# Performance work log

Hardware: AMD Instinct MI355X
Metric: run time of the kernel (lower is better)

## Reference

```python
import jax, jax.numpy as jnp
import numpy as np

B, V, D, H, E = 512, 128, 256, 4, 2
Dh = D // H

def setup_inputs() -> dict:
    key = jax.random.key(0)
    k = jax.random.split(key, 8)
    x = jax.random.normal(k[0], (B, V, D), dtype=jnp.float32)
    adj = jax.random.randint(k[1], (V, V), 0, 2, dtype=jnp.int32)
    adj = adj.at[jnp.arange(V), jnp.arange(V)].set(1)  # self loops so no empty columns for real nodes
    edge_attr = jax.random.normal(k[2], (V, V, E), dtype=jnp.float32)
    mask = jax.random.bernoulli(k[3], 0.1, (B, V))  # True = padded view
    # learned params (torch Linear: y = x @ W.T)
    W = jax.random.normal(k[4], (D, D), dtype=jnp.float32) / np.sqrt(D)
    a = jax.random.normal(k[5], (2 * Dh,), dtype=jnp.float32) / np.sqrt(2 * Dh)  # attn.weight flattened
    Ew = jax.random.normal(k[6], (H, E), dtype=jnp.float32) / np.sqrt(E)  # edge_proj.weight
    return {"x": x, "adj": adj, "edge_attr": edge_attr, "mask": mask, "W": W, "a": a, "Ew": Ew}

def reference(x, adj, edge_attr, mask, W, a, Ew):
    Bv, Vv, Dv = x.shape
    Hh = Ew.shape[0]
    Dhh = Dv // Hh
    Wx = (x @ W.T).reshape(Bv, Vv, Hh, Dhh)                 # [B,V,H,Dh]
    a_src, a_dst = a[:Dhh], a[Dhh:]
    s_src = jnp.einsum('bvhd,d->bvh', Wx, a_src)             # a^T[Wh_i ; .]
    s_dst = jnp.einsum('bvhd,d->bvh', Wx, a_dst)             # a^T[. ; Wh_j]
    ef = jnp.einsum('ije,he->ijh', edge_attr, Ew)            # [V,V,H]
    e = s_src[:, :, None, :] + s_dst[:, None, :, :] + ef[None]  # [B,i,j,H]
    e = jnp.where(e >= 0, e, 0.2 * e)                        # leaky_relu(0.2)
    valid = (adj.astype(bool))[None, :, :, None] & (~mask)[:, :, None, None] & (~mask)[:, None, :, None]
    e = jnp.where(valid, e, -jnp.inf)
    # softmax over source dim i (axis=1), safe for all-masked columns (-> 0, like nan_to_num)
    m = jnp.max(e, axis=1, keepdims=True)
    m = jnp.where(jnp.isfinite(m), m, 0.0)
    p = jnp.where(valid, jnp.exp(e - m), 0.0)
    denom = jnp.sum(p, axis=1, keepdims=True)
    alpha = p / jnp.where(denom == 0, 1.0, denom)            # [B,i,j,H]
    h = jnp.einsum('bijh,bihd->bjhd', alpha, Wx).reshape(Bv, Vv, Dv)
    h = jax.nn.elu(h)
    return jnp.where(mask[:, :, None], 0.0, h)
```

## Files before the change

kernel.cpp:

```cpp
#include <hip/hip_runtime.h>
#include <cmath>

#define BB 512
#define VV 128
#define DD 256
#define HH 4
#define DHH 64

typedef unsigned short u16;
typedef __attribute__((ext_vector_type(8))) short bf16x8;
typedef __attribute__((ext_vector_type(4))) short bf16x4;
typedef __attribute__((ext_vector_type(4))) float f32x4;

__device__ __forceinline__ u16 f2bf(float f) {
    unsigned u = __builtin_bit_cast(unsigned, f);
    u = (u + 0x7fffu + ((u >> 16) & 1u)) >> 16;
    return (u16)u;
}

__global__ void k_ef(const float* __restrict__ ea, const float* __restrict__ Ew,
                     const int* __restrict__ adj, float* __restrict__ efm) {
    int idx = blockIdx.x * 256 + threadIdx.x;
    int hh = idx >> 14, ij = idx & 16383;
    float v = -INFINITY;
    if (adj[ij])
        v = fmaf(ea[ij * 2 + 1], Ew[hh * 2 + 1], ea[ij * 2] * Ew[hh * 2]);
    efm[idx] = v;
}

__global__ __launch_bounds__(256, 2) void k_gemm(
    const float* __restrict__ x, const float* __restrict__ Wm,
    const float* __restrict__ a, u16* __restrict__ WxT,
    float* __restrict__ s_src, float* __restrict__ s_dst) {
    __shared__ u16 As[128 * 32];
    __shared__ u16 Bs[128 * 32];

    const int t = threadIdx.x;
    const int w = t >> 6, L = t & 63;
    const int wr = w >> 1, wc = w & 1;
    const int lr = L & 15, lg = L >> 4;
    const int b  = blockIdx.x;
    const int c0 = blockIdx.y * 128;
    const int row = t >> 1, seg = t & 1;

    f32x4 acc[4][4];
    #pragma unroll
    for (int i = 0; i < 4; ++i)
        #pragma unroll
        for (int j = 0; j < 4; ++j) acc[i][j] = (f32x4){0.f, 0.f, 0.f, 0.f};

    const float* xrow = x  + (size_t)(b * 128 + row) * DD + seg * 16;
    const float* wrow = Wm + (size_t)(c0 + row) * DD + seg * 16;
    u16* adst = &As[row * 32 + seg * 16];
    u16* bdst = &Bs[row * 32 + seg * 16];

    for (int k0 = 0; k0 < DD; k0 += 32) {
        float4 f0 = *(const float4*)(xrow + k0);
        float4 f1 = *(const float4*)(xrow + k0 + 4);
        float4 f2 = *(const float4*)(xrow + k0 + 8);
        float4 f3 = *(const float4*)(xrow + k0 + 12);
        float4 g0 = *(const float4*)(wrow + k0);
        float4 g1 = *(const float4*)(wrow + k0 + 4);
        float4 g2 = *(const float4*)(wrow + k0 + 8);
        float4 g3 = *(const float4*)(wrow + k0 + 12);
        bf16x8 pa, pb, qa, qb;
        pa[0]=(short)f2bf(f0.x); pa[1]=(short)f2bf(f0.y); pa[2]=(short)f2bf(f0.z); pa[3]=(short)f2bf(f0.w);
        pa[4]=(short)f2bf(f1.x); pa[5]=(short)f2bf(f1.y); pa[6]=(short)f2bf(f1.z); pa[7]=(short)f2bf(f1.w);
        pb[0]=(short)f2bf(f2.x); pb[1]=(short)f2bf(f2.y); pb[2]=(short)f2bf(f2.z); pb[3]=(short)f2bf(f2.w);
        pb[4]=(short)f2bf(f3.x); pb[5]=(short)f2bf(f3.y); pb[6]=(short)f2bf(f3.z); pb[7]=(short)f2bf(f3.w);
        qa[0]=(short)f2bf(g0.x); qa[1]=(short)f2bf(g0.y); qa[2]=(short)f2bf(g0.z); qa[3]=(short)f2bf(g0.w);
        qa[4]=(short)f2bf(g1.x); qa[5]=(short)f2bf(g1.y); qa[6]=(short)f2bf(g1.z); qa[7]=(short)f2bf(g1.w);
        qb[0]=(short)f2bf(g2.x); qb[1]=(short)f2bf(g2.y); qb[2]=(short)f2bf(g2.z); qb[3]=(short)f2bf(g2.w);
        qb[4]=(short)f2bf(g3.x); qb[5]=(short)f2bf(g3.y); qb[6]=(short)f2bf(g3.z); qb[7]=(short)f2bf(g3.w);
        *(bf16x8*)adst       = pa;
        *(bf16x8*)(adst + 8) = pb;
        *(bf16x8*)bdst       = qa;
        *(bf16x8*)(bdst + 8) = qb;
        __syncthreads();

        bf16x8 af[4], bfr[4];
        #pragma unroll
        for (int mi = 0; mi < 4; ++mi)
            af[mi] = *(const bf16x8*)&As[(wr * 64 + mi * 16 + lr) * 32 + lg * 8];
        #pragma unroll
        for (int ni = 0; ni < 4; ++ni)
            bfr[ni] = *(const bf16x8*)&Bs[(wc * 64 + ni * 16 + lr) * 32 + lg * 8];
        #pragma unroll
        for (int mi = 0; mi < 4; ++mi)
            #pragma unroll
            for (int ni = 0; ni < 4; ++ni)
                acc[mi][ni] = __builtin_amdgcn_mfma_f32_16x16x32_bf16(
                    af[mi], bfr[ni], acc[mi][ni], 0, 0, 0);
        __syncthreads();
    }

    const int h = blockIdx.y * 2 + wc;
    float as_[4], ad_[4];
    #pragma unroll
    for (int ni = 0; ni < 4; ++ni) {
        as_[ni] = a[ni * 16 + lr];
        ad_[ni] = a[64 + ni * 16 + lr];
    }
    float ps[16], pd[16];
    #pragma unroll
    for (int k = 0; k < 16; ++k) { ps[k] = 0.f; pd[k] = 0.f; }

    #pragma unroll
    for (int mi = 0; mi < 4; ++mi) {
        #pragma unroll
        for (int ni = 0; ni < 4; ++ni) {
            int d  = ni * 16 + lr;
            int vb = wr * 64 + mi * 16 + lg * 4;
            bf16x4 o;
            #pragma unroll
            for (int r = 0; r < 4; ++r) {
                float v = acc[mi][ni][r];
                o[r] = (short)f2bf(v);
                ps[mi * 4 + r] = fmaf(v, as_[ni], ps[mi * 4 + r]);
                pd[mi * 4 + r] = fmaf(v, ad_[ni], pd[mi * 4 + r]);
            }
            *(bf16x4*)&WxT[(((size_t)b * HH + h) * DHH + d) * VV + vb] = o;
        }
    }
    #pragma unroll
    for (int k = 0; k < 16; ++k) {
        #pragma unroll
        for (int m = 1; m < 16; m <<= 1) {
            ps[k] += __shfl_xor(ps[k], m);
            pd[k] += __shfl_xor(pd[k], m);
        }
    }
    if (lr == 0) {
        #pragma unroll
        for (int mi = 0; mi < 4; ++mi)
            #pragma unroll
            for (int r = 0; r < 4; ++r) {
                int v = wr * 64 + mi * 16 + lg * 4 + r;
                s_src[((size_t)b * VV + v) * HH + h] = ps[mi * 4 + r];
                s_dst[((size_t)b * VV + v) * HH + h] = pd[mi * 4 + r];
            }
    }
}

__global__ __launch_bounds__(256, 4) void k_attn(
    const u16* __restrict__ WxT, const float* __restrict__ s_src,
    const float* __restrict__ s_dst, const float* __restrict__ efm,
    const int* __restrict__ mask, float* __restrict__ out) {
    __shared__ u16 alT[128 * 136];
    __shared__ float ssl[128], sdl[128], red[256], rden[128];

    const int t = threadIdx.x;
    const int b = blockIdx.x >> 2, h = blockIdx.x & 3;

    if (t < 128) {
        int mk = mask[b * VV + t];
        float vs = s_src[((size_t)b * VV + t) * HH + h];
        float vd = s_dst[((size_t)b * VV + t) * HH + h];
        ssl[t] = mk ? -INFINITY : vs;
        sdl[t] = mk ? -INFINITY : vd;
    }
    __syncthreads();

    const int j = t & 127, half = t >> 7;
    const float sdj = sdl[j];
    const float* efh = efm + ((size_t)h * VV + half * 64) * VV + j;
    float psum = 0.f;
    for (int i8 = 0; i8 < 64; i8 += 8) {
        bf16x8 pk;
        #pragma unroll
        for (int u = 0; u < 8; ++u) {
            int i = half * 64 + i8 + u;
            float e = ssl[i] + sdj + efh[(size_t)(i8 + u) * VV];
            e = e >= 0.f ? e : 0.2f * e;
            float p = __expf(e);
            psum += p;
            pk[u] = (short)f2bf(p);
        }
        *(bf16x8*)&alT[j * 136 + half * 64 + i8] = pk;
    }
    red[half * 128 + j] = psum;
    __syncthreads();
    if (half == 0) {
        float s = red[j] + red[128 + j];
        rden[j] = s > 0.f ? 1.f / s : 0.f;
    }
    __syncthreads();

    const int w = t >> 6, L = t & 63;
    const int lr = L & 15, lg = L >> 4;
    const u16* gB = WxT + ((size_t)b * HH + h) * DHH * VV;
    f32x4 acc[2][4];
    #pragma unroll
    for (int mi = 0; mi < 2; ++mi)
        #pragma unroll
        for (int ni = 0; ni < 4; ++ni) acc[mi][ni] = (f32x4){0.f, 0.f, 0.f, 0.f};

    #pragma unroll
    for (int ks = 0; ks < 4; ++ks) {
        const int kk = ks * 32 + lg * 8;
        bf16x8 bfr[4];
        #pragma unroll
        for (int ni = 0; ni < 4; ++ni)
            bfr[ni] = *(const bf16x8*)(gB + (size_t)(ni * 16 + lr) * VV + kk);
        #pragma unroll
        for (int mi = 0; mi < 2; ++mi) {
            bf16x8 af = *(const bf16x8*)&alT[(w * 32 + mi * 16 + lr) * 136 + kk];
            #pragma unroll
            for (int ni = 0; ni < 4; ++ni)
                acc[mi][ni] = __builtin_amdgcn_mfma_f32_16x16x32_bf16(
                    af, bfr[ni], acc[mi][ni], 0, 0, 0);
        }
    }

    #pragma unroll
    for (int mi = 0; mi < 2; ++mi)
        #pragma unroll
        for (int ni = 0; ni < 4; ++ni) {
            int dcol = ni * 16 + lr;
            int jb   = w * 32 + mi * 16 + lg * 4;
            float* op = out + ((size_t)b * VV + jb) * DD + h * DHH + dcol;
            #pragma unroll
            for (int r = 0; r < 4; ++r) {
                float v = acc[mi][ni][r] * rden[jb + r];
                v = v > 0.f ? v : expm1f(v);
                op[(size_t)r * DD] = v;
            }
        }
}

extern "C" void kernel_launch(void* const* d_in, const int* in_sizes, int n_in,
                              void* d_out, int out_size, void* d_ws, size_t ws_size,
                              hipStream_t stream) {
    const float* x    = (const float*)d_in[0];
    const int*   adj  = (const int*)d_in[1];
    const float* ea   = (const float*)d_in[2];
    const int*   mask = (const int*)d_in[3];
    const float* Wm   = (const float*)d_in[4];
    const float* a    = (const float*)d_in[5];
    const float* Ew   = (const float*)d_in[6];
    float* out = (float*)d_out;

    u16*   WxT   = (u16*)d_ws;
    float* s_src = (float*)(WxT + (size_t)BB * HH * DHH * VV);
    float* s_dst = s_src + (size_t)BB * VV * HH;
    float* efm   = s_dst + (size_t)BB * VV * HH;

    k_ef<<<HH * VV * VV / 256, 256, 0, stream>>>(ea, Ew, adj, efm);
    k_gemm<<<dim3(BB, 2), 256, 0, stream>>>(x, Wm, a, WxT, s_src, s_dst);
    k_attn<<<BB * HH, 256, 0, stream>>>(WxT, s_src, s_dst, efm, mask, out);
}
```

Before: 168.5 us.

## Fuse projection GEMM and attention into one kernel keeping Wx in LDS

Merges the projection GEMM and the attention kernel into one kernel per (batch, head-pair). The bf16 Wx tile and the attention scores now stay in shared memory instead of going through global memory, which removes the WxT/s_src/s_dst global round trip and one launch. It also register-prefetches the next K slice of x/W during the MFMA loop and pads the LDS rows (stride 40) to reduce bank conflicts. The cost is much larger LDS use per block (about 70KB), which may limit occupancy, and fewer blocks (1024 instead of 2048) for the attention phase.

```diff
diff --git a/kernel.cpp b/kernel.cpp
--- a/kernel.cpp
+++ b/kernel.cpp
@@ -16,6 +16,9 @@
     unsigned u = __builtin_bit_cast(unsigned, f);
     u = (u + 0x7fffu + ((u >> 16) & 1u)) >> 16;
     return (u16)u;
+}
+__device__ __forceinline__ unsigned pk2(float a, float b) {
+    return (unsigned)f2bf(a) | ((unsigned)f2bf(b) << 16);
 }
 
 __global__ void k_ef(const float* __restrict__ ea, const float* __restrict__ Ew,
@@ -28,20 +31,32 @@
     efm[idx] = v;
 }
 
-__global__ __launch_bounds__(256, 2) void k_gemm(
+__global__ __launch_bounds__(256, 2) void k_fused(
     const float* __restrict__ x, const float* __restrict__ Wm,
-    const float* __restrict__ a, u16* __restrict__ WxT,
-    float* __restrict__ s_src, float* __restrict__ s_dst) {
-    __shared__ u16 As[128 * 32];
-    __shared__ u16 Bs[128 * 32];
+    const float* __restrict__ a, const float* __restrict__ efm,
+    const int* __restrict__ mask, float* __restrict__ out) {
+    __shared__ u16 WxL[128 * 136];
+    __shared__ u16 scratch[128 * 136];
+    __shared__ float ssl[256], sdl[256], red[256], rden[128];
+    __shared__ int mkl[128];
+
+    u16* As = scratch;
+    u16* Bs = scratch + 128 * 40;
+    u16* alT = scratch;
 
     const int t = threadIdx.x;
+    const int b = blockIdx.x, hp = blockIdx.y;
     const int w = t >> 6, L = t & 63;
     const int wr = w >> 1, wc = w & 1;
     const int lr = L & 15, lg = L >> 4;
-    const int b  = blockIdx.x;
-    const int c0 = blockIdx.y * 128;
+
+    if (t < 128) mkl[t] = mask[b * VV + t];
+
     const int row = t >> 1, seg = t & 1;
+    const float* xs = x  + ((size_t)b * VV + row) * DD + seg * 16;
+    const float* ws = Wm + ((size_t)(hp * 128 + row)) * DD + seg * 16;
+    u16* adst = As + row * 40 + seg * 16;
+    u16* bdst = Bs + row * 40 + seg * 16;
 
     f32x4 acc[4][4];
     #pragma unroll
@@ -49,42 +64,44 @@
         #pragma unroll
         for (int j = 0; j < 4; ++j) acc[i][j] = (f32x4){0.f, 0.f, 0.f, 0.f};
 
-    const float* xrow = x  + (size_t)(b * 128 + row) * DD + seg * 16;
-    const float* wrow = Wm + (size_t)(c0 + row) * DD + seg * 16;
-    u16* adst = &As[row * 32 + seg * 16];
-    u16* bdst = &Bs[row * 32 + seg * 16];
-
-    for (int k0 = 0; k0 < DD; k0 += 32) {
-        float4 f0 = *(const float4*)(xrow + k0);
-        float4 f1 = *(const float4*)(xrow + k0 + 4);
-        float4 f2 = *(const float4*)(xrow + k0 + 8);
-        float4 f3 = *(const float4*)(xrow + k0 + 12);
-        float4 g0 = *(const float4*)(wrow + k0);
-        float4 g1 = *(const float4*)(wrow + k0 + 4);
-        float4 g2 = *(const float4*)(wrow + k0 + 8);
-        float4 g3 = *(const float4*)(wrow + k0 + 12);
-        bf16x8 pa, pb, qa, qb;
-        pa[0]=(short)f2bf(f0.x); pa[1]=(short)f2bf(f0.y); pa[2]=(short)f2bf(f0.z); pa[3]=(short)f2bf(f0.w);
-        pa[4]=(short)f2bf(f1.x); pa[5]=(short)f2bf(f1.y); pa[6]=(short)f2bf(f1.z); pa[7]=(short)f2bf(f1.w);
-        pb[0]=(short)f2bf(f2.x); pb[1]=(short)f2bf(f2.y); pb[2]=(short)f2bf(f2.z); pb[3]=(short)f2bf(f2.w);
-        pb[4]=(short)f2bf(f3.x); pb[5]=(short)f2bf(f3.y); pb[6]=(short)f2bf(f3.z); pb[7]=(short)f2bf(f3.w);
-        qa[0]=(short)f2bf(g0.x); qa[1]=(short)f2bf(g0.y); qa[2]=(short)f2bf(g0.z); qa[3]=(short)f2bf(g0.w);
-        qa[4]=(short)f2bf(g1.x); qa[5]=(short)f2bf(g1.y); qa[6]=(short)f2bf(g1.z); qa[7]=(short)f2bf(g1.w);
-        qb[0]=(short)f2bf(g2.x); qb[1]=(short)f2bf(g2.y); qb[2]=(short)f2bf(g2.z); qb[3]=(short)f2bf(g2.w);
-        qb[4]=(short)f2bf(g3.x); qb[5]=(short)f2bf(g3.y); qb[6]=(short)f2bf(g3.z); qb[7]=(short)f2bf(g3.w);
-        *(bf16x8*)adst       = pa;
-        *(bf16x8*)(adst + 8) = pb;
+    float4 px[4], pw[4];
+    #pragma unroll
+    for (int q = 0; q < 4; ++q) {
+        px[q] = *(const float4*)(xs + q * 4);
+        pw[q] = *(const float4*)(ws + q * 4);
+    }
+
+    for (int ks = 0; ks < 8; ++ks) {
+        bf16x8 va, vb, qa, qb;
+        unsigned* vap = (unsigned*)&va; unsigned* vbp = (unsigned*)&vb;
+        unsigned* qap = (unsigned*)&qa; unsigned* qbp = (unsigned*)&qb;
+        vap[0] = pk2(px[0].x, px[0].y); vap[1] = pk2(px[0].z, px[0].w);
+        vap[2] = pk2(px[1].x, px[1].y); vap[3] = pk2(px[1].z, px[1].w);
+        vbp[0] = pk2(px[2].x, px[2].y); vbp[1] = pk2(px[2].z, px[2].w);
+        vbp[2] = pk2(px[3].x, px[3].y); vbp[3] = pk2(px[3].z, px[3].w);
+        qap[0] = pk2(pw[0].x, pw[0].y); qap[1] = pk2(pw[0].z, pw[0].w);
+        qap[2] = pk2(pw[1].x, pw[1].y); qap[3] = pk2(pw[1].z, pw[1].w);
+        qbp[0] = pk2(pw[2].x, pw[2].y); qbp[1] = pk2(pw[2].z, pw[2].w);
+        qbp[2] = pk2(pw[3].x, pw[3].y); qbp[3] = pk2(pw[3].z, pw[3].w);
+        *(bf16x8*)adst       = va;
+        *(bf16x8*)(adst + 8) = vb;
         *(bf16x8*)bdst       = qa;
         *(bf16x8*)(bdst + 8) = qb;
         __syncthreads();
-
+        if (ks < 7) {
+            #pragma unroll
+            for (int q = 0; q < 4; ++q) {
+                px[q] = *(const float4*)(xs + (ks + 1) * 32 + q * 4);
+                pw[q] = *(const float4*)(ws + (ks + 1) * 32 + q * 4);
+            }
+        }
         bf16x8 af[4], bfr[4];
         #pragma unroll
         for (int mi = 0; mi < 4; ++mi)
-            af[mi] = *(const bf16x8*)&As[(wr * 64 + mi * 16 + lr) * 32 + lg * 8];
+            af[mi] = *(const bf16x8*)&As[(wr * 64 + mi * 16 + lr) * 40 + lg * 8];
         #pragma unroll
         for (int ni = 0; ni < 4; ++ni)
-            bfr[ni] = *(const bf16x8*)&Bs[(wc * 64 + ni * 16 + lr) * 32 + lg * 8];
+            bfr[ni] = *(const bf16x8*)&Bs[(wc * 64 + ni * 16 + lr) * 40 + lg * 8];
         #pragma unroll
         for (int mi = 0; mi < 4; ++mi)
             #pragma unroll
@@ -94,7 +111,6 @@
         __syncthreads();
     }
 
-    const int h = blockIdx.y * 2 + wc;
     float as_[4], ad_[4];
     #pragma unroll
     for (int ni = 0; ni < 4; ++ni) {
@@ -104,13 +120,12 @@
     float ps[16], pd[16];
     #pragma unroll
     for (int k = 0; k < 16; ++k) { ps[k] = 0.f; pd[k] = 0.f; }
-
     #pragma unroll
     for (int mi = 0; mi < 4; ++mi) {
         #pragma unroll
         for (int ni = 0; ni < 4; ++ni) {
-            int d  = ni * 16 + lr;
-            int vb = wr * 64 + mi * 16 + lg * 4;
+            const int c  = wc * 64 + ni * 16 + lr;
+            const int vb = wr * 64 + mi * 16 + lg * 4;
             bf16x4 o;
             #pragma unroll
             for (int r = 0; r < 4; ++r) {
@@ -119,7 +134,7 @@
                 ps[mi * 4 + r] = fmaf(v, as_[ni], ps[mi * 4 + r]);
                 pd[mi * 4 + r] = fmaf(v, ad_[ni], pd[mi * 4 + r]);
             }
-            *(bf16x4*)&WxT[(((size_t)b * HH + h) * DHH + d) * VV + vb] = o;
+            *(bf16x4*)&WxL[c * 136 + vb] = o;
         }
     }
     #pragma unroll
@@ -136,96 +151,78 @@
             #pragma unroll
             for (int r = 0; r < 4; ++r) {
                 int v = wr * 64 + mi * 16 + lg * 4 + r;
-                s_src[((size_t)b * VV + v) * HH + h] = ps[mi * 4 + r];
-                s_dst[((size_t)b * VV + v) * HH + h] = pd[mi * 4 + r];
-            }
-    }
-}
-
-__global__ __launch_bounds__(256, 4) void k_attn(
-    const u16* __restrict__ WxT, const float* __restrict__ s_src,
-    const float* __restrict__ s_dst, const float* __restrict__ efm,
-    const int* __restrict__ mask, float* __restrict__ out) {
-    __shared__ u16 alT[128 * 136];
-    __shared__ float ssl[128], sdl[128], red[256], rden[128];
-
-    const int t = threadIdx.x;
-    const int b = blockIdx.x >> 2, h = blockIdx.x & 3;
-
-    if (t < 128) {
-        int mk = mask[b * VV + t];
-        float vs = s_src[((size_t)b * VV + t) * HH + h];
-        float vd = s_dst[((size_t)b * VV + t) * HH + h];
-        ssl[t] = mk ? -INFINITY : vs;
-        sdl[t] = mk ? -INFINITY : vd;
+                bool mk = mkl[v] != 0;
+                ssl[wc * 128 + v] = mk ? -INFINITY : ps[mi * 4 + r];
+                sdl[wc * 128 + v] = mk ? -INFINITY : pd[mi * 4 + r];
+            }
     }
     __syncthreads();
 
     const int j = t & 127, half = t >> 7;
-    const float sdj = sdl[j];
-    const float* efh = efm + ((size_t)h * VV + half * 64) * VV + j;
-    float psum = 0.f;
-    for (int i8 = 0; i8 < 64; i8 += 8) {
-        bf16x8 pk;
-        #pragma unroll
-        for (int u = 0; u < 8; ++u) {
-            int i = half * 64 + i8 + u;
-            float e = ssl[i] + sdj + efh[(size_t)(i8 + u) * VV];
-            e = e >= 0.f ? e : 0.2f * e;
-            float p = __expf(e);
-            psum += p;
-            pk[u] = (short)f2bf(p);
-        }
-        *(bf16x8*)&alT[j * 136 + half * 64 + i8] = pk;
-    }
-    red[half * 128 + j] = psum;
-    __syncthreads();
-    if (half == 0) {
-        float s = red[j] + red[128 + j];
-        rden[j] = s > 0.f ? 1.f / s : 0.f;
-    }
-    __syncthreads();
-
-    const int w = t >> 6, L = t & 63;
-    const int lr = L & 15, lg = L >> 4;
-    const u16* gB = WxT + ((size_t)b * HH + h) * DHH * VV;
-    f32x4 acc[2][4];
-    #pragma unroll
-    for (int mi = 0; mi < 2; ++mi)
-        #pragma unroll
-        for (int ni = 0; ni < 4; ++ni) acc[mi][ni] = (f32x4){0.f, 0.f, 0.f, 0.f};
-
-    #pragma unroll
-    for (int ks = 0; ks < 4; ++ks) {
-        const int kk = ks * 32 + lg * 8;
-        bf16x8 bfr[4];
-        #pragma unroll
-        for (int ni = 0; ni < 4; ++ni)
-            bfr[ni] = *(const bf16x8*)(gB + (size_t)(ni * 16 + lr) * VV + kk);
-        #pragma unroll
-        for (int mi = 0; mi < 2; ++mi) {
-            bf16x8 af = *(const bf16x8*)&alT[(w * 32 + mi * 16 + lr) * 136 + kk];
+    for (int hl = 0; hl < 2; ++hl) {
+        const int h = hp * 2 + hl;
+        const float sdj = sdl[hl * 128 + j];
+        const float* efh = efm + ((size_t)h * VV + half * 64) * VV + j;
+        u16* alrow = alT + j * 136 + half * 64;
+        float psum = 0.f;
+        for (int i8 = 0; i8 < 64; i8 += 8) {
+            bf16x8 pk;
+            #pragma unroll
+            for (int u = 0; u < 8; ++u) {
+                float e = ssl[hl * 128 + half * 64 + i8 + u] + sdj
+                        + efh[(size_t)(i8 + u) * VV];
+                e = e >= 0.f ? e : 0.2f * e;
+                float p = __expf(e);
+                psum += p;
+                pk[u] = (short)f2bf(p);
+            }
+            *(bf16x8*)(alrow + i8) = pk;
+        }
+        red[half * 128 + j] = psum;
+        __syncthreads();
+        if (half == 0) {
+            float s = red[j] + red[128 + j];
+            rden[j] = s > 0.f ? 1.f / s : 0.f;
+        }
+        __syncthreads();
+
+        f32x4 acc2[2][4];
+        #pragma unroll
+        for (int mi = 0; mi < 2; ++mi)
+            #pragma unroll
+            for (int ni = 0; ni < 4; ++ni) acc2[mi][ni] = (f32x4){0.f, 0.f, 0.f, 0.f};
+        #pragma unroll
+        for (int ks = 0; ks < 4; ++ks) {
+            const int kk = ks * 32 + lg * 8;
+            bf16x8 bfr2[4];
             #pragma unroll
             for (int ni = 0; ni < 4; ++ni)
-                acc[mi][ni] = __builtin_amdgcn_mfma_f32_16x16x32_bf16(
-                    af, bfr[ni], acc[mi][ni], 0, 0, 0);
-        }
-    }
-
-    #pragma unroll
-    for (int mi = 0; mi < 2; ++mi)
-        #pragma unroll
-        for (int ni = 0; ni < 4; ++ni) {
-            int dcol = ni * 16 + lr;
-            int jb   = w * 32 + mi * 16 + lg * 4;
-            float* op = out + ((size_t)b * VV + jb) * DD + h * DHH + dcol;
-            #pragma unroll
-            for (int r = 0; r < 4; ++r) {
-                float v = acc[mi][ni][r] * rden[jb + r];
-                v = v > 0.f ? v : expm1f(v);
-                op[(size_t)r * DD] = v;
-            }
-        }
+                bfr2[ni] = *(const bf16x8*)&WxL[(hl * 64 + ni * 16 + lr) * 136 + kk];
+            #pragma unroll
+            for (int mi = 0; mi < 2; ++mi) {
+                bf16x8 af2 = *(const bf16x8*)&alT[(w * 32 + mi * 16 + lr) * 136 + kk];
+                #pragma unroll
+                for (int ni = 0; ni < 4; ++ni)
+                    acc2[mi][ni] = __builtin_amdgcn_mfma_f32_16x16x32_bf16(
+                        af2, bfr2[ni], acc2[mi][ni], 0, 0, 0);
+            }
+        }
+        #pragma unroll
+        for (int mi = 0; mi < 2; ++mi)
+            #pragma unroll
+            for (int ni = 0; ni < 4; ++ni) {
+                const int dcol = ni * 16 + lr;
+                const int jb   = w * 32 + mi * 16 + lg * 4;
+                float* op = out + ((size_t)b * VV + jb) * DD + h * DHH + dcol;
+                #pragma unroll
+                for (int r = 0; r < 4; ++r) {
+                    float v = acc2[mi][ni][r] * rden[jb + r];
+                    v = v > 0.f ? v : expm1f(v);
+                    op[(size_t)r * DD] = v;
+                }
+            }
+        __syncthreads();
+    }
 }
 
 extern "C" void kernel_launch(void* const* d_in, const int* in_sizes, int n_in,
@@ -240,12 +237,8 @@
     const float* Ew   = (const float*)d_in[6];
     float* out = (float*)d_out;
 
-    u16*   WxT   = (u16*)d_ws;
-    float* s_src = (float*)(WxT + (size_t)BB * HH * DHH * VV);
-    float* s_dst = s_src + (size_t)BB * VV * HH;
-    float* efm   = s_dst + (size_t)BB * VV * HH;
+    float* efm = (float*)d_ws;
 
     k_ef<<<HH * VV * VV / 256, 256, 0, stream>>>(ea, Ew, adj, efm);
-    k_gemm<<<dim3(BB, 2), 256, 0, stream>>>(x, Wm, a, WxT, s_src, s_dst);
-    k_attn<<<BB * HH, 256, 0, stream>>>(WxT, s_src, s_dst, efm, mask, out);
-}
+    k_fused<<<dim3(BB, 2), 256, 0, stream>>>(x, Wm, a, efm, mask, out);
+}
```

Result: no change. 166.3 us (-1.3%).
